# Kernel tuning notes

Hardware: AMD Instinct MI355X
Metric: run time of the kernel (lower is better)

The kernel has to match this reference:

```python
import jax, jax.numpy as jnp
import numpy as np

B, N, D, H = 2, 2048, 768, 12
HD = D // H  # head_dim = 64
SCALE = HD ** -0.5


def setup_inputs() -> dict:
    key = jax.random.key(0)
    ks = jax.random.split(key, 8)
    return {
        "x": jax.random.normal(ks[0], (B, N, D), jnp.float32),
        "masks": jax.random.uniform(ks[1], (B, H, N), jnp.float32),
        "lambda_r": jax.random.uniform(ks[2], (B, H), jnp.float32) * 4.0 + 1.0,
        "theta_r": jax.random.uniform(ks[3], (B, H), jnp.float32),
        "mask_weights": jax.random.uniform(ks[4], (B, H), jnp.float32),
        "qkv_w": jax.random.normal(ks[5], (D, 3 * D), jnp.float32) * (D ** -0.5),
        "qkv_b": jnp.zeros((3 * D,), jnp.float32),
        "proj_w": jax.random.normal(ks[6], (D, D), jnp.float32) * (D ** -0.5),
        "proj_b": jnp.zeros((D,), jnp.float32),
    }


def reference(x, masks, lambda_r, theta_r, mask_weights, qkv_w, qkv_b, proj_w, proj_b):
    # qkv projection: [B,N,3D] -> [3,B,H,N,HD]
    qkv = (x @ qkv_w + qkv_b).reshape(B, N, 3, H, HD).transpose(2, 0, 3, 1, 4)
    q, k, v = qkv[0], qkv[1], qkv[2]
    # raw scores [B,H,N,N]
    attn = jnp.einsum('bhqd,bhkd->bhqk', q, k) * SCALE
    # region gate: sigmoid(lambda * (m_i*m_j - theta)) multiplied into scores pre-softmax
    gate = jax.nn.sigmoid(
        lambda_r[:, :, None, None]
        * (masks[:, :, :, None] * masks[:, :, None, :] - theta_r[:, :, None, None])
    )
    attn = jax.nn.softmax(attn * gate, axis=-1)  # dropout is identity in eval
    out = jnp.einsum('bhqk,bhkd->bqhd', attn, v).reshape(B, N, D)
    # per-head output scaling via mask_weights
    out = out * jnp.repeat(mask_weights, HD, axis=-1)[:, None, :]
    return out @ proj_w + proj_b
```

## Files before the change

kernel.cpp:

```cpp
#include <hip/hip_runtime.h>

typedef unsigned short u16;
typedef unsigned int u32;
typedef __attribute__((ext_vector_type(8))) short short8;
typedef __attribute__((ext_vector_type(4))) float f32x4;

#define NB 2
#define NSEQ 2048
#define DIM 768
#define NH 12
#define HDIM 64

#define LOG2E 1.44269504088896f
#define CFOLD 0.18033688f

#if defined(__has_builtin)
#if __has_builtin(__builtin_amdgcn_exp2f)
#define EXPB(x) __builtin_amdgcn_exp2f(x)
#else
#define EXPB(x) exp2f(x)
#endif
#if __has_builtin(__builtin_amdgcn_rcpf)
#define RCP(x) __builtin_amdgcn_rcpf(x)
#else
#define RCP(x) (1.0f / (x))
#endif
#else
#define EXPB(x) exp2f(x)
#define RCP(x) (1.0f / (x))
#endif

__device__ __forceinline__ u16 f2bf(float x) {
    union { float f; unsigned u; } v; v.f = x;
    unsigned r = v.u + 0x7fffu + ((v.u >> 16) & 1u);
    return (u16)(r >> 16);
}

__device__ __forceinline__ u32 pack_bf16(float a, float b) {
    union { float f; u32 u; } A, B; A.f = a; B.f = b;
    u32 ra = A.u + 0x7fffu + ((A.u >> 16) & 1u);
    u32 rb = B.u + 0x7fffu + ((B.u >> 16) & 1u);
    return __builtin_amdgcn_perm(rb, ra, 0x07060302u);
}

__device__ __forceinline__ u32 pack_rtn(float a, float b) {
    union { float f; u32 u; } A, B; A.f = a; B.f = b;
    return __builtin_amdgcn_perm(B.u + 0x8000u, A.u + 0x8000u, 0x07060302u);
}

__device__ __forceinline__ f32x4 mfma16(short8 a, short8 b, f32x4 c) {
    return __builtin_amdgcn_mfma_f32_16x16x32_bf16(a, b, c, 0, 0, 0);
}

__device__ __forceinline__ void glds16(const u16* g, u16* l) {
    __builtin_amdgcn_global_load_lds((const __attribute__((address_space(1))) u32*)g,
                                     (__attribute__((address_space(3))) u32*)l, 16, 0, 0);
}

__global__ __launch_bounds__(256) void prep(const float* __restrict__ x, u16* __restrict__ xb,
                                            const float* __restrict__ qkv_w, u16* __restrict__ wq,
                                            const float* __restrict__ proj_w, u16* __restrict__ wp) {
    const int t = threadIdx.x;
    int bid = blockIdx.x;
    if (bid < 3072) {
        int i = (bid * 256 + t) * 4;
        float4 v = *(const float4*)(x + i);
        *(uint2*)(xb + i) = make_uint2(pack_bf16(v.x, v.y), pack_bf16(v.z, v.w));
        return;
    }
    const float* in; u16* outp; int rows, cols, bx, by;
    if (bid < 3072 + 1728) {
        bid -= 3072; in = qkv_w; outp = wq; rows = 768; cols = 2304;
        bx = bid % 72; by = bid / 72;
    } else {
        bid -= 4800; in = proj_w; outp = wp; rows = 768; cols = 768;
        bx = bid % 24; by = bid / 24;
    }
    __shared__ float tile[32][33];
    int c0 = bx * 32, r0 = by * 32;
    int tx = t & 31, ty = t >> 5;
    #pragma unroll
    for (int i = 0; i < 32; i += 8)
        tile[ty + i][tx] = in[(size_t)(r0 + ty + i) * cols + c0 + tx];
    __syncthreads();
    #pragma unroll
    for (int i = 0; i < 32; i += 8)
        outp[(size_t)(c0 + ty + i) * rows + r0 + tx] = f2bf(tile[tx][ty + i]);
}

__global__ __launch_bounds__(256) void vtrans(const u16* __restrict__ vin,
                                              u16* __restrict__ vout) {
    __shared__ __align__(16) u16 tile[64][72];
    const int bh = blockIdx.y;
    const int n0 = blockIdx.x * 64;
    const int t = threadIdx.x;
    const size_t base = (size_t)bh * NSEQ * HDIM;
    int r = t >> 3, cb = (t & 7) * 8;
    *(uint4*)&tile[r][cb]      = *(const uint4*)&vin[base + (size_t)(n0 + r) * HDIM + cb];
    *(uint4*)&tile[r + 32][cb] = *(const uint4*)&vin[base + (size_t)(n0 + r + 32) * HDIM + cb];
    __syncthreads();
    #pragma unroll
    for (int half = 0; half < 2; half++) {
        int d = (t >> 3) + half * 32;
        int nb = (t & 7) * 8;
        short8 v;
        #pragma unroll
        for (int j = 0; j < 8; j++) v[j] = (short)tile[nb + j][d];
        *(short8*)&vout[base + (size_t)d * NSEQ + n0 + nb] = v;
    }
}

__global__ __launch_bounds__(256) void gemm_qkv(const u16* __restrict__ A,
                                                const u16* __restrict__ BT,
                                                const float* __restrict__ bias,
                                                u16* __restrict__ qo,
                                                u16* __restrict__ ko,
                                                u16* __restrict__ vo) {
    __shared__ __align__(16) u16 As[128 * 32];
    __shared__ __align__(16) u16 Bs[128 * 32];
    const int bm = blockIdx.y * 128, bn = blockIdx.x * 128;
    const int t = threadIdx.x;
    const int lane = t & 63, wave = t >> 6;
    const int l15 = lane & 15, quad = lane >> 4;
    const int wm = (wave >> 1) * 64, wn = (wave & 1) * 64;

    const u16* ga = A + (size_t)(bm + (t >> 2)) * DIM + (t & 3) * 8;
    const u16* gb = BT + (size_t)(bn + (t >> 2)) * DIM + (t & 3) * 8;
    u16* la = As + wave * 512;
    u16* lb = Bs + wave * 512;

    f32x4 acc[4][4] = {};
    for (int k0 = 0; k0 < DIM; k0 += 32) {
        __syncthreads();
        glds16(ga, la);
        glds16(ga + (size_t)64 * DIM, la + 2048);
        glds16(gb, lb);
        glds16(gb + (size_t)64 * DIM, lb + 2048);
        ga += 32; gb += 32;
        __syncthreads();
        short8 af[4], bf[4];
        #pragma unroll
        for (int i = 0; i < 4; i++) af[i] = *(const short8*)&As[(wm + i * 16 + l15) * 32 + quad * 8];
        #pragma unroll
        for (int j = 0; j < 4; j++) bf[j] = *(const short8*)&Bs[(wn + j * 16 + l15) * 32 + quad * 8];
        #pragma unroll
        for (int i = 0; i < 4; i++)
            #pragma unroll
            for (int j = 0; j < 4; j++)
                acc[i][j] = mfma16(af[i], bf[j], acc[i][j]);
    }

    #pragma unroll
    for (int i = 0; i < 4; i++) {
        int mr = bm + wm + i * 16 + quad * 4;
        int b = mr >> 11, nn = mr & 2047;
        #pragma unroll
        for (int j = 0; j < 4; j++) {
            int ncol = bn + wn + j * 16 + l15;
            int w = ncol / DIM, rem = ncol - w * DIM;
            int h = rem >> 6, hd = rem & 63;
            u16* dst = (w == 0) ? qo : (w == 1) ? ko : vo;
            float bb = bias[ncol];
            size_t idx = (((size_t)(b * NH + h)) * NSEQ + nn) * HDIM + hd;
            #pragma unroll
            for (int r = 0; r < 4; r++)
                dst[idx + (size_t)r * HDIM] = f2bf(acc[i][j][r] + bb);
        }
    }
}

__global__ __launch_bounds__(512) void attn_kernel(const u16* __restrict__ Q,
                                                   const u16* __restrict__ Kg,
                                                   const u16* __restrict__ Vt,
                                                   const float* __restrict__ masks,
                                                   const float* __restrict__ lambda_r,
                                                   const float* __restrict__ theta_r,
                                                   const float* __restrict__ mask_w,
                                                   u16* __restrict__ AO) {
    const int bh = blockIdx.y;
    const int b = bh / NH, h = bh % NH;
    const int qb = blockIdx.x * 64;
    const int t = threadIdx.x, wave = t >> 6, lane = t & 63;
    const int l15 = lane & 15, quad = lane >> 4;
    const int g = wave >> 1, kh = wave & 1;

    __shared__ __align__(16) u16 pool[16384];
    __shared__ __align__(16) u16 Ps[8][640];
    __shared__ __align__(16) float mks[2][64];
    __shared__ float Ls[8][16];

    const float lam = lambda_r[bh], th = theta_r[bh], mw = mask_w[bh];
    const float Bfac = lam * th * LOG2E;

    const size_t base = (size_t)bh * (NSEQ * HDIM);
    const int qrow = qb + g * 16;

    const u16* Qr = Q + base + (size_t)(qrow + l15) * HDIM;
    short8 bq0 = *(const short8*)(Qr + quad * 8);
    short8 bq1 = *(const short8*)(Qr + 32 + quad * 8);
    const float Afac = -lam * LOG2E * masks[bh * NSEQ + qrow + l15];

    const int srow = t >> 3;
    const int gc = (t & 7) ^ (srow & 7);
    const u16* kgp = Kg + base + (size_t)srow * HDIM + gc * 8;
    const u16* vgp = Vt + base + (size_t)srow * NSEQ + gc * 8;
    const int wbase = wave * 512;

    const int ph = (quad ^ (l15 & 7)) * 8;
    const int vph = kh ? (ph ^ 32) : ph;
    u16* PsW = Ps[wave];
    const int pw = l15 * 40 + quad * 4;
    const int prd = l15 * 40 + quad * 8;
    const float* mrow = masks + bh * NSEQ;

    float lsum = 0.f;
    f32x4 O[4] = {};

    glds16(kgp, pool + wbase);
    glds16(vgp, pool + 8192 + wbase);
    if (t < 16) *(float4*)&mks[0][t * 4] = *(const float4*)&mrow[t * 4];

    const int NT = NSEQ / 64;
    for (int kt = 0; kt < NT; kt++) {
        const int bufofs = (kt & 1) * 4096;
        __syncthreads();
        if (kt + 1 < NT) {
            glds16(kgp + (kt + 1) * 64 * HDIM, pool + (bufofs ^ 4096) + wbase);
            glds16(vgp + (kt + 1) * 64, pool + 8192 + (bufofs ^ 4096) + wbase);
            if (t < 16) *(float4*)&mks[(kt + 1) & 1][t * 4] =
                *(const float4*)&mrow[(kt + 1) * 64 + t * 4];
        }
        const u16* KsB = pool + bufofs;
        const u16* VsB = pool + 8192 + bufofs;
        const float* mkb = mks[kt & 1];

        float gp[2][4];
        #pragma unroll
        for (int c = 0; c < 2; c++) {
            float4 mkv = *(const float4*)&mkb[kh * 32 + c * 16 + quad * 4];
            #pragma unroll
            for (int r = 0; r < 4; r++) {
                float mk = (r == 0) ? mkv.x : (r == 1) ? mkv.y : (r == 2) ? mkv.z : mkv.w;
                float e = EXPB(fmaf(mk, Afac, Bfac));
                gp[c][r] = CFOLD * RCP(1.0f + e);
            }
        }

        #pragma unroll
        for (int c = 0; c < 2; c++) {
            const int krow = kh * 32 + c * 16 + l15;
            short8 ak0 = *(const short8*)&KsB[krow * 64 + ph];
            short8 ak1 = *(const short8*)&KsB[krow * 64 + (ph ^ 32)];
            f32x4 S = {0.f, 0.f, 0.f, 0.f};
            S = mfma16(ak0, bq0, S);
            S = mfma16(ak1, bq1, S);
            float p[4];
            #pragma unroll
            for (int r = 0; r < 4; r++) p[r] = EXPB(S[r] * gp[c][r]);
            lsum += (p[0] + p[1]) + (p[2] + p[3]);
            *(uint2*)&PsW[pw + c * 16] = make_uint2(pack_rtn(p[0], p[1]), pack_rtn(p[2], p[3]));
        }

        short8 bp = *(const short8*)&PsW[prd];
        #pragma unroll
        for (int dt = 0; dt < 4; dt++) {
            short8 av = *(const short8*)&VsB[(dt * 16 + l15) * 64 + vph];
            O[dt] = mfma16(av, bp, O[dt]);
        }
    }

    __syncthreads();
    float* Op = (float*)pool;
    const int slot = (wave * 64 + lane) * 16;
    #pragma unroll
    for (int dt = 0; dt < 4; dt++) *(f32x4*)&Op[slot + dt * 4] = O[dt];
    float ls = lsum;
    ls += __shfl_xor(ls, 16);
    ls += __shfl_xor(ls, 32);
    if (quad == 0) Ls[wave][l15] = ls;
    __syncthreads();
    if (kh == 0) {
        const int pslot = ((wave ^ 1) * 64 + lane) * 16;
        float sc = mw / (ls + Ls[wave ^ 1][l15]);
        u16* aor = AO + ((size_t)(b * NSEQ) + qrow + l15) * DIM + h * HDIM + quad * 4;
        #pragma unroll
        for (int dt = 0; dt < 4; dt++) {
            f32x4 oc = *(const f32x4*)&Op[pslot + dt * 4];
            float o0 = (O[dt][0] + oc[0]) * sc, o1 = (O[dt][1] + oc[1]) * sc;
            float o2 = (O[dt][2] + oc[2]) * sc, o3 = (O[dt][3] + oc[3]) * sc;
            *(uint2*)(aor + dt * 16) = make_uint2(pack_rtn(o0, o1), pack_rtn(o2, o3));
        }
    }
}

__global__ __launch_bounds__(256) void gemm_proj(const u16* __restrict__ A,
                                                 const u16* __restrict__ BT,
                                                 const float* __restrict__ bias,
                                                 float* __restrict__ outp) {
    __shared__ __align__(16) u16 As[128 * 32];
    __shared__ __align__(16) u16 Bs[64 * 32];
    const int bm = blockIdx.y * 128, bn = blockIdx.x * 64;
    const int t = threadIdx.x;
    const int lane = t & 63, wave = t >> 6;
    const int l15 = lane & 15, quad = lane >> 4;
    const int wm = wave * 32;

    const u16* ga = A + (size_t)(bm + (t >> 2)) * DIM + (t & 3) * 8;
    const u16* gb = BT + (size_t)(bn + (t >> 2)) * DIM + (t & 3) * 8;
    u16* la = As + wave * 512;
    u16* lb = Bs + wave * 512;

    f32x4 acc[2][4] = {};
    for (int k0 = 0; k0 < DIM; k0 += 32) {
        __syncthreads();
        glds16(ga, la);
        glds16(ga + (size_t)64 * DIM, la + 2048);
        glds16(gb, lb);
        ga += 32; gb += 32;
        __syncthreads();
        short8 af[2], bf[4];
        #pragma unroll
        for (int i = 0; i < 2; i++) af[i] = *(const short8*)&As[(wm + i * 16 + l15) * 32 + quad * 8];
        #pragma unroll
        for (int j = 0; j < 4; j++) bf[j] = *(const short8*)&Bs[(j * 16 + l15) * 32 + quad * 8];
        #pragma unroll
        for (int i = 0; i < 2; i++)
            #pragma unroll
            for (int j = 0; j < 4; j++)
                acc[i][j] = mfma16(af[i], bf[j], acc[i][j]);
    }

    #pragma unroll
    for (int i = 0; i < 2; i++) {
        int mr = bm + wm + i * 16 + quad * 4;
        #pragma unroll
        for (int j = 0; j < 4; j++) {
            int ncol = bn + j * 16 + l15;
            float bb = bias[ncol];
            #pragma unroll
            for (int r = 0; r < 4; r++)
                outp[(size_t)(mr + r) * DIM + ncol] = acc[i][j][r] + bb;
        }
    }
}

extern "C" void kernel_launch(void* const* d_in, const int* in_sizes, int n_in,
                              void* d_out, int out_size, void* d_ws, size_t ws_size,
                              hipStream_t stream) {
    const float* x            = (const float*)d_in[0];
    const float* masks        = (const float*)d_in[1];
    const float* lambda_r     = (const float*)d_in[2];
    const float* theta_r      = (const float*)d_in[3];
    const float* mask_weights = (const float*)d_in[4];
    const float* qkv_w        = (const float*)d_in[5];
    const float* qkv_b        = (const float*)d_in[6];
    const float* proj_w       = (const float*)d_in[7];
    const float* proj_b       = (const float*)d_in[8];
    float* outp = (float*)d_out;

    const size_t SZH = (size_t)NB * NH * NSEQ * HDIM;
    u16* xb    = (u16*)d_ws;
    u16* wqkvT = xb + (size_t)4096 * 768;
    u16* wprT  = wqkvT + (size_t)2304 * 768;
    u16* qg    = wprT + (size_t)768 * 768;
    u16* kg    = qg + SZH;
    u16* vtmp  = kg + SZH;
    u16* vt    = vtmp + SZH;
    u16* ao    = xb;

    prep<<<dim3(3072 + 1728 + 576), 256, 0, stream>>>(x, xb, qkv_w, wqkvT, proj_w, wprT);
    gemm_qkv<<<dim3(2304 / 128, 4096 / 128), 256, 0, stream>>>(xb, wqkvT, qkv_b, qg, kg, vtmp);
    vtrans<<<dim3(NSEQ / 64, NB * NH), 256, 0, stream>>>(vtmp, vt);
    attn_kernel<<<dim3(NSEQ / 64, NB * NH), 512, 0, stream>>>(qg, kg, vt, masks, lambda_r,
                                                              theta_r, mask_weights, ao);
    gemm_proj<<<dim3(768 / 64, 4096 / 128), 256, 0, stream>>>(ao, wprT, proj_b, outp);
}
```

Before: 187.2 us.

## Keep P in registers via 16x16x16 MFMA, drop LDS P staging and mask buffer

The attention inner loop no longer writes the probability tile to shared memory and reads it back. It feeds the packed bf16 P fragments straight into 16x16x16 bf16 MFMAs, reading V with a matching swizzled layout. The softmax scale constant is folded into Q during the QKV projection epilogue. Key masks are prefetched into registers per lane instead of through an LDS double buffer, and packing uses the hardware cvt_pk_bf16 instruction when available. This removes LDS round-trips and a shared buffer, at the cost of twice as many smaller-K MFMA instructions for PV.

```diff
diff --git a/kernel.cpp b/kernel.cpp
--- a/kernel.cpp
+++ b/kernel.cpp
@@ -3,6 +3,7 @@
 typedef unsigned short u16;
 typedef unsigned int u32;
 typedef __attribute__((ext_vector_type(8))) short short8;
+typedef __attribute__((ext_vector_type(4))) short short4v;
 typedef __attribute__((ext_vector_type(4))) float f32x4;
 
 #define NB 2
@@ -48,8 +49,22 @@
     return __builtin_amdgcn_perm(B.u + 0x8000u, A.u + 0x8000u, 0x07060302u);
 }
 
+#if defined(__has_builtin) && __has_builtin(__builtin_amdgcn_cvt_pk_bf16_f32)
+__device__ __forceinline__ u32 pkbf(float a, float b) {
+    auto r = __builtin_amdgcn_cvt_pk_bf16_f32(a, b);
+    union { __typeof__(r) v; u32 u; } c; c.v = r;
+    return c.u;
+}
+#else
+#define pkbf pack_rtn
+#endif
+
 __device__ __forceinline__ f32x4 mfma16(short8 a, short8 b, f32x4 c) {
     return __builtin_amdgcn_mfma_f32_16x16x32_bf16(a, b, c, 0, 0, 0);
+}
+
+__device__ __forceinline__ f32x4 mfma1k(short4v a, short4v b, f32x4 c) {
+    return __builtin_amdgcn_mfma_f32_16x16x16bf16_1k(a, b, c, 0, 0, 0);
 }
 
 __device__ __forceinline__ void glds16(const u16* g, u16* l) {
@@ -150,6 +165,7 @@
                 acc[i][j] = mfma16(af[i], bf[j], acc[i][j]);
     }
 
+    const float cscale = (bn < DIM) ? CFOLD : 1.0f;
     #pragma unroll
     for (int i = 0; i < 4; i++) {
         int mr = bm + wm + i * 16 + quad * 4;
@@ -164,7 +180,7 @@
             size_t idx = (((size_t)(b * NH + h)) * NSEQ + nn) * HDIM + hd;
             #pragma unroll
             for (int r = 0; r < 4; r++)
-                dst[idx + (size_t)r * HDIM] = f2bf(acc[i][j][r] + bb);
+                dst[idx + (size_t)r * HDIM] = f2bf((acc[i][j][r] + bb) * cscale);
         }
     }
 }
@@ -185,8 +201,6 @@
     const int g = wave >> 1, kh = wave & 1;
 
     __shared__ __align__(16) u16 pool[16384];
-    __shared__ __align__(16) u16 Ps[8][640];
-    __shared__ __align__(16) float mks[2][64];
     __shared__ float Ls[8][16];
 
     const float lam = lambda_r[bh], th = theta_r[bh], mw = mask_w[bh];
@@ -207,10 +221,13 @@
     const int wbase = wave * 512;
 
     const int ph = (quad ^ (l15 & 7)) * 8;
-    const int vph = kh ? (ph ^ 32) : ph;
-    u16* PsW = Ps[wave];
-    const int pw = l15 * 40 + quad * 4;
-    const int prd = l15 * 40 + quad * 8;
+    const int krow0 = (kh * 32 + l15) * 64;
+    const int krow1 = (kh * 32 + 16 + l15) * 64;
+    const int vsw = l15 & 7;
+    const int vrow = l15 * 64 + (quad & 1) * 4;
+    const int vch0 = ((kh * 4 + (quad >> 1)) ^ vsw) * 8;
+    const int vch1 = ((kh * 4 + 2 + (quad >> 1)) ^ vsw) * 8;
+
     const float* mrow = masks + bh * NSEQ;
 
     float lsum = 0.f;
@@ -218,55 +235,62 @@
 
     glds16(kgp, pool + wbase);
     glds16(vgp, pool + 8192 + wbase);
-    if (t < 16) *(float4*)&mks[0][t * 4] = *(const float4*)&mrow[t * 4];
+    float4 mk0 = *(const float4*)&mrow[kh * 32 + quad * 4];
+    float4 mk1 = *(const float4*)&mrow[kh * 32 + 16 + quad * 4];
 
     const int NT = NSEQ / 64;
     for (int kt = 0; kt < NT; kt++) {
         const int bufofs = (kt & 1) * 4096;
         __syncthreads();
+        float4 nk0 = mk0, nk1 = mk1;
         if (kt + 1 < NT) {
             glds16(kgp + (kt + 1) * 64 * HDIM, pool + (bufofs ^ 4096) + wbase);
             glds16(vgp + (kt + 1) * 64, pool + 8192 + (bufofs ^ 4096) + wbase);
-            if (t < 16) *(float4*)&mks[(kt + 1) & 1][t * 4] =
-                *(const float4*)&mrow[(kt + 1) * 64 + t * 4];
+            nk0 = *(const float4*)&mrow[(kt + 1) * 64 + kh * 32 + quad * 4];
+            nk1 = *(const float4*)&mrow[(kt + 1) * 64 + kh * 32 + 16 + quad * 4];
         }
         const u16* KsB = pool + bufofs;
         const u16* VsB = pool + 8192 + bufofs;
-        const float* mkb = mks[kt & 1];
-
-        float gp[2][4];
-        #pragma unroll
-        for (int c = 0; c < 2; c++) {
-            float4 mkv = *(const float4*)&mkb[kh * 32 + c * 16 + quad * 4];
-            #pragma unroll
-            for (int r = 0; r < 4; r++) {
-                float mk = (r == 0) ? mkv.x : (r == 1) ? mkv.y : (r == 2) ? mkv.z : mkv.w;
-                float e = EXPB(fmaf(mk, Afac, Bfac));
-                gp[c][r] = CFOLD * RCP(1.0f + e);
-            }
+
+        float gp0[4], gp1[4];
+        gp0[0] = RCP(1.0f + EXPB(fmaf(mk0.x, Afac, Bfac)));
+        gp0[1] = RCP(1.0f + EXPB(fmaf(mk0.y, Afac, Bfac)));
+        gp0[2] = RCP(1.0f + EXPB(fmaf(mk0.z, Afac, Bfac)));
+        gp0[3] = RCP(1.0f + EXPB(fmaf(mk0.w, Afac, Bfac)));
+        gp1[0] = RCP(1.0f + EXPB(fmaf(mk1.x, Afac, Bfac)));
+        gp1[1] = RCP(1.0f + EXPB(fmaf(mk1.y, Afac, Bfac)));
+        gp1[2] = RCP(1.0f + EXPB(fmaf(mk1.z, Afac, Bfac)));
+        gp1[3] = RCP(1.0f + EXPB(fmaf(mk1.w, Afac, Bfac)));
+
+        short8 a00 = *(const short8*)&KsB[krow0 + ph];
+        short8 a01 = *(const short8*)&KsB[krow0 + (ph ^ 32)];
+        short8 a10 = *(const short8*)&KsB[krow1 + ph];
+        short8 a11 = *(const short8*)&KsB[krow1 + (ph ^ 32)];
+        f32x4 S0 = {0.f, 0.f, 0.f, 0.f}, S1 = {0.f, 0.f, 0.f, 0.f};
+        S0 = mfma16(a00, bq0, S0);
+        S1 = mfma16(a10, bq0, S1);
+        S0 = mfma16(a01, bq1, S0);
+        S1 = mfma16(a11, bq1, S1);
+
+        float p0[4], p1[4];
+        #pragma unroll
+        for (int r = 0; r < 4; r++) p0[r] = EXPB(S0[r] * gp0[r]);
+        #pragma unroll
+        for (int r = 0; r < 4; r++) p1[r] = EXPB(S1[r] * gp1[r]);
+        lsum += (p0[0] + p0[1]) + (p0[2] + p0[3]) + (p1[0] + p1[1]) + (p1[2] + p1[3]);
+        union { uint2 u; short4v s; } c0, c1;
+        c0.u = make_uint2(pkbf(p0[0], p0[1]), pkbf(p0[2], p0[3]));
+        c1.u = make_uint2(pkbf(p1[0], p1[1]), pkbf(p1[2], p1[3]));
+
+        #pragma unroll
+        for (int dt = 0; dt < 4; dt++) {
+            short4v av0 = *(const short4v*)&VsB[vrow + dt * 1024 + vch0];
+            short4v av1 = *(const short4v*)&VsB[vrow + dt * 1024 + vch1];
+            O[dt] = mfma1k(av0, c0.s, O[dt]);
+            O[dt] = mfma1k(av1, c1.s, O[dt]);
         }
 
-        #pragma unroll
-        for (int c = 0; c < 2; c++) {
-            const int krow = kh * 32 + c * 16 + l15;
-            short8 ak0 = *(const short8*)&KsB[krow * 64 + ph];
-            short8 ak1 = *(const short8*)&KsB[krow * 64 + (ph ^ 32)];
-            f32x4 S = {0.f, 0.f, 0.f, 0.f};
-            S = mfma16(ak0, bq0, S);
-            S = mfma16(ak1, bq1, S);
-            float p[4];
-            #pragma unroll
-            for (int r = 0; r < 4; r++) p[r] = EXPB(S[r] * gp[c][r]);
-            lsum += (p[0] + p[1]) + (p[2] + p[3]);
-            *(uint2*)&PsW[pw + c * 16] = make_uint2(pack_rtn(p[0], p[1]), pack_rtn(p[2], p[3]));
-        }
-
-        short8 bp = *(const short8*)&PsW[prd];
-        #pragma unroll
-        for (int dt = 0; dt < 4; dt++) {
-            short8 av = *(const short8*)&VsB[(dt * 16 + l15) * 64 + vph];
-            O[dt] = mfma16(av, bp, O[dt]);
-        }
+        mk0 = nk0; mk1 = nk1;
     }
 
     __syncthreads();
```

Result: slower. 194.1 us (+3.7%).
